# Kernel optimization log

Measured on AMD Instinct MI355X. Metric: run time of the kernel, lower is better.

Reference implementation:

```python
import jax, jax.numpy as jnp
import numpy as np

N = 50000       # nodes
E = 600000      # edges (avg degree 12)
F_IN = 64       # input_bands
F_HID = 128     # 2 * input_bands
F_OUT = 128     # output_bands
EPS = 1e-5      # BatchNorm eps


def setup_inputs() -> dict:
    key = jax.random.key(0)
    ks = jax.random.split(key, 12)
    x = jax.random.normal(ks[0], (N, F_IN), jnp.float32)
    edge_index = jax.random.randint(ks[1], (2, E), 0, N, dtype=jnp.int32)
    # GCNConv weight (glorot-ish) and bias
    W1 = jax.random.normal(ks[2], (F_IN, F_HID), jnp.float32) / np.sqrt(F_IN)
    b1 = jnp.zeros((F_HID,), jnp.float32)
    gamma1 = jnp.ones((F_HID,), jnp.float32)
    beta1 = jnp.zeros((F_HID,), jnp.float32)
    # SAGEConv: lin_l (aggregated neighbors, with bias), lin_r (root, no bias)
    Wl = jax.random.normal(ks[3], (F_HID, F_OUT), jnp.float32) / np.sqrt(F_HID)
    bl = jnp.zeros((F_OUT,), jnp.float32)
    Wr = jax.random.normal(ks[4], (F_HID, F_OUT), jnp.float32) / np.sqrt(F_HID)
    gamma2 = jnp.ones((F_OUT,), jnp.float32)
    beta2 = jnp.zeros((F_OUT,), jnp.float32)
    return {"x": x, "edge_index": edge_index, "W1": W1, "b1": b1,
            "gamma1": gamma1, "beta1": beta1, "Wl": Wl, "bl": bl,
            "Wr": Wr, "gamma2": gamma2, "beta2": beta2}


def _bn_train(h, gamma, beta):
    # BatchNorm1d in training mode: biased batch stats over the node axis
    mean = h.mean(axis=0)
    var = h.var(axis=0)
    return gamma * (h - mean) * jax.lax.rsqrt(var + EPS) + beta


def _gcn_conv(x, src, dst, W, b):
    # PyG GCNConv: x' = D^{-1/2}(A + I)D^{-1/2} X W + b
    h = x @ W                                   # [N, F_HID]
    loop = jnp.arange(N, dtype=src.dtype)
    src_sl = jnp.concatenate([src, loop])       # self-loops appended
    dst_sl = jnp.concatenate([dst, loop])
    deg = jax.ops.segment_sum(jnp.ones(E + N, h.dtype), dst_sl, num_segments=N)
    dis = jnp.where(deg > 0, jax.lax.rsqrt(deg), 0.0)  # deg^{-1/2}, inf -> 0
    norm = dis[src_sl] * dis[dst_sl]            # [E+N]
    msg = h[src_sl] * norm[:, None]             # gather + scale
    return jax.ops.segment_sum(msg, dst_sl, num_segments=N) + b


def _sage_conv(x, src, dst, Wl, bl, Wr):
    # PyG SAGEConv (mean aggr): x' = lin_l(mean_{j in N(i)} x_j) + lin_r(x_i)
    cnt = jax.ops.segment_sum(jnp.ones(E, x.dtype), dst, num_segments=N)
    neigh = jax.ops.segment_sum(x[src], dst, num_segments=N)
    neigh = neigh / jnp.maximum(cnt, 1.0)[:, None]
    return neigh @ Wl + bl + x @ Wr


def reference(x, edge_index, W1, b1, gamma1, beta1, Wl, bl, Wr, gamma2, beta2):
    src, dst = edge_index[0], edge_index[1]
    h = _gcn_conv(x, src, dst, W1, b1)
    h = jax.nn.relu(_bn_train(h, gamma1, beta1))  # dropout = identity (eval)
    h = _sage_conv(h, src, dst, Wl, bl, Wr)
    h = jax.nn.relu(_bn_train(h, gamma2, beta2))
    return h
```

## Files before the change

### kernel.cpp

```cpp
#include <hip/hip_runtime.h>


#define NN 50000
#define NE 600000
#define FIN 64
#define FHID 128
#define BN_EPS 1e-5f
#define CAP 64
#define NSLOT 32

typedef __attribute__((ext_vector_type(8))) short short8;
typedef __attribute__((ext_vector_type(4))) float f32x4;

__device__ __forceinline__ unsigned short f2bf(float f) {
  unsigned u = __float_as_uint(f);
  return (unsigned short)((u + 0x7FFFu + ((u >> 16) & 1u)) >> 16);
}
__device__ __forceinline__ float bfs(unsigned short u) {
  return __uint_as_float(((unsigned)u) << 16);
}
__device__ __forceinline__ float bflo(unsigned v) { return __uint_as_float(v << 16); }
__device__ __forceinline__ float bfhi(unsigned v) { return __uint_as_float(v & 0xFFFF0000u); }
__device__ __forceinline__ unsigned pk2(float lo, float hi) {
  return (unsigned)f2bf(lo) | ((unsigned)f2bf(hi) << 16);
}

__global__ __launch_bounds__(256) void bucket_fill(
    const int* __restrict__ src, const int* __restrict__ dst,
    int* __restrict__ cnt, int* __restrict__ csr,
    const float* __restrict__ W1, const float* __restrict__ Wl,
    const float* __restrict__ Wr, short* __restrict__ Wp1,
    short* __restrict__ Wp2, int nbE4) {
  int tid = threadIdx.x;
  if ((int)blockIdx.x < nbE4) {
    int e4 = blockIdx.x * 256 + tid;
    if (e4 * 4 < NE) {
      int4 d4 = ((const int4*)dst)[e4];
      int4 s4 = ((const int4*)src)[e4];
      int p;
      p = atomicAdd(&cnt[d4.x], 1); if (p < CAP) csr[(size_t)d4.x * CAP + p] = s4.x;
      p = atomicAdd(&cnt[d4.y], 1); if (p < CAP) csr[(size_t)d4.y * CAP + p] = s4.y;
      p = atomicAdd(&cnt[d4.z], 1); if (p < CAP) csr[(size_t)d4.z * CAP + p] = s4.z;
      p = atomicAdd(&cnt[d4.w], 1); if (p < CAP) csr[(size_t)d4.w * CAP + p] = s4.w;
    }
  } else {
    int widx = (blockIdx.x - nbE4) * 256 + tid;
    if (widx < 8192) {
      int kk = widx & 7, lane = (widx >> 3) & 63, ks = (widx >> 9) & 1,
          n = widx >> 10;
      int q = lane >> 4, r = lane & 15;
      int k = ks * 32 + q * 8 + kk, col = n * 16 + r;
      Wp1[widx] = (short)f2bf(W1[k * 128 + col]);
    } else if (widx < 8192 + 32768) {
      int w2 = widx - 8192;
      int kk = w2 & 7, lane = (w2 >> 3) & 63, ks = (w2 >> 9) & 7, n = w2 >> 12;
      int q = lane >> 4, r = lane & 15;
      int k = ks * 32 + q * 8 + kk, col = n * 16 + r;
      float wv = (k < 128) ? Wl[k * 128 + col] : Wr[(k - 128) * 128 + col];
      Wp2[w2] = (short)f2bf(wv);
    }
  }
}

__global__ __launch_bounds__(256) void scale_x(const float* __restrict__ x,
                                               const int* __restrict__ cnt,
                                               ushort4* __restrict__ xs,
                                               int* __restrict__ csr) {
  int i = blockIdx.x * 256 + threadIdx.x;
  float4 v = ((const float4*)x)[i];
  int node = i >> 4;
  float d = rsqrtf((float)(cnt[node] + 1));
  xs[i] = make_ushort4(f2bf(v.x * d), f2bf(v.y * d), f2bf(v.z * d), f2bf(v.w * d));
  if (i < NN) {
    int deg = min(cnt[i], CAP);
    int deg8 = (deg + 7) & ~7;
    int* cb = csr + (size_t)i * CAP;
    for (int p = deg; p < deg8; ++p) cb[p] = 0;
  }
}

__device__ __forceinline__ void gacc(float& a0, float& a1, float& a2, float& a3,
                                     ushort4 v) {
  a0 += bfs(v.x); a1 += bfs(v.y); a2 += bfs(v.z); a3 += bfs(v.w);
}

__global__ __launch_bounds__(256) void gcn_block(
    const unsigned short* __restrict__ xs, const int* __restrict__ csr,
    const int* __restrict__ cnt, const short* __restrict__ Wp1,
    const float* __restrict__ b1, unsigned short* __restrict__ hb,
    float* __restrict__ sums1s, float* __restrict__ sumsq1s) {
  __shared__ unsigned short xaS[16][72];
  __shared__ float lsum[128], lsq[128];
  int tid = threadIdx.x;
  if (tid < 128) { lsum[tid] = 0.f; lsq[tid] = 0.f; }
  int row_base = blockIdx.x * 16;
  int li = tid & 15, g = tid >> 4;
  int node = row_base + g;
  {
    int degr = cnt[node];
    int deg = min(degr, CAP);
    int deg8 = (deg + 7) & ~7;
    float di = rsqrtf((float)(degr + 1));
    ushort4 sv = *(const ushort4*)(xs + (size_t)node * FIN + li * 4);
    float a0 = bfs(sv.x), a1 = bfs(sv.y), a2 = bfs(sv.z), a3 = bfs(sv.w);
    ushort4 zv = *(const ushort4*)(xs + li * 4);
    const int* cb = csr + (size_t)node * CAP;
    int4 sA = *(const int4*)(cb);
    int4 sB = *(const int4*)(cb + 4);
    for (int e = 0; e < deg8; e += 8) {
      int pn = min(e + 8, CAP - 8);
      int4 nA = *(const int4*)(cb + pn);
      int4 nB = *(const int4*)(cb + pn + 4);
      ushort4 v0 = *(const ushort4*)(xs + (size_t)sA.x * FIN + li * 4);
      ushort4 v1 = *(const ushort4*)(xs + (size_t)sA.y * FIN + li * 4);
      ushort4 v2 = *(const ushort4*)(xs + (size_t)sA.z * FIN + li * 4);
      ushort4 v3 = *(const ushort4*)(xs + (size_t)sA.w * FIN + li * 4);
      ushort4 v4 = *(const ushort4*)(xs + (size_t)sB.x * FIN + li * 4);
      ushort4 v5 = *(const ushort4*)(xs + (size_t)sB.y * FIN + li * 4);
      ushort4 v6 = *(const ushort4*)(xs + (size_t)sB.z * FIN + li * 4);
      ushort4 v7 = *(const ushort4*)(xs + (size_t)sB.w * FIN + li * 4);
      gacc(a0, a1, a2, a3, v0); gacc(a0, a1, a2, a3, v1);
      gacc(a0, a1, a2, a3, v2); gacc(a0, a1, a2, a3, v3);
      gacc(a0, a1, a2, a3, v4); gacc(a0, a1, a2, a3, v5);
      gacc(a0, a1, a2, a3, v6); gacc(a0, a1, a2, a3, v7);
      sA = nA; sB = nB;
    }
    float pc = (float)(deg8 - deg);
    a0 -= pc * bfs(zv.x); a1 -= pc * bfs(zv.y);
    a2 -= pc * bfs(zv.z); a3 -= pc * bfs(zv.w);
    *(ushort4*)(&xaS[g][li * 4]) = make_ushort4(
        f2bf(di * a0), f2bf(di * a1), f2bf(di * a2), f2bf(di * a3));
  }
  __syncthreads();

  int lane = tid & 63, w = tid >> 6, r = lane & 15, q = lane >> 4;
  int n0 = w * 2, n1 = w * 2 + 1;
  short8 af0 = *(const short8*)(&xaS[r][q * 8]);
  short8 af1 = *(const short8*)(&xaS[r][32 + q * 8]);
  f32x4 acc0 = (f32x4){0.f, 0.f, 0.f, 0.f}, acc1 = acc0;
  acc0 = __builtin_amdgcn_mfma_f32_16x16x32_bf16(
      af0, *(const short8*)(Wp1 + ((size_t)(n0 * 2 + 0) * 64 + lane) * 8), acc0, 0, 0, 0);
  acc1 = __builtin_amdgcn_mfma_f32_16x16x32_bf16(
      af0, *(const short8*)(Wp1 + ((size_t)(n1 * 2 + 0) * 64 + lane) * 8), acc1, 0, 0, 0);
  acc0 = __builtin_amdgcn_mfma_f32_16x16x32_bf16(
      af1, *(const short8*)(Wp1 + ((size_t)(n0 * 2 + 1) * 64 + lane) * 8), acc0, 0, 0, 0);
  acc1 = __builtin_amdgcn_mfma_f32_16x16x32_bf16(
      af1, *(const short8*)(Wp1 + ((size_t)(n1 * 2 + 1) * 64 + lane) * 8), acc1, 0, 0, 0);

  float b0 = b1[n0 * 16 + r], bb1 = b1[n1 * 16 + r];
  float cs0 = 0.f, cq0 = 0.f, cs1 = 0.f, cq1 = 0.f;
#pragma unroll
  for (int i = 0; i < 4; ++i) {
    int row = row_base + q * 4 + i;
    float v0 = acc0[i] + b0;
    float v1 = acc1[i] + bb1;
    hb[(size_t)row * 128 + n0 * 16 + r] = f2bf(v0);
    hb[(size_t)row * 128 + n1 * 16 + r] = f2bf(v1);
    cs0 += v0; cq0 += v0 * v0;
    cs1 += v1; cq1 += v1 * v1;
  }
  atomicAdd(&lsum[n0 * 16 + r], cs0);
  atomicAdd(&lsq[n0 * 16 + r], cq0);
  atomicAdd(&lsum[n1 * 16 + r], cs1);
  atomicAdd(&lsq[n1 * 16 + r], cq1);
  __syncthreads();
  if (tid < 128) {
    int s = blockIdx.x & (NSLOT - 1);
    atomicAdd(&sums1s[s * 128 + tid], lsum[tid]);
    atomicAdd(&sumsq1s[s * 128 + tid], lsq[tid]);
  }
}

__global__ __launch_bounds__(256) void bn_slot_apply_bf(
    unsigned* __restrict__ hb, const float* __restrict__ sums1s,
    const float* __restrict__ sumsq1s, const float* __restrict__ gamma,
    const float* __restrict__ beta) {
  __shared__ float sc[128], sh[128];
  int t = threadIdx.x;
  if (t < 128) {
    float ms = 0.f, vs = 0.f;
#pragma unroll
    for (int s = 0; s < NSLOT; ++s) {
      ms += sums1s[s * 128 + t];
      vs += sumsq1s[s * 128 + t];
    }
    float mean = ms * (1.0f / NN);
    float var = fmaxf(vs * (1.0f / NN) - mean * mean, 0.f);
    float sgm = gamma[t] * rsqrtf(var + BN_EPS);
    sc[t] = sgm;
    sh[t] = beta[t] - mean * sgm;
  }
  __syncthreads();
  for (int i = blockIdx.x * 256 + t; i < NN * FHID / 4; i += gridDim.x * 256) {
    uint2 v = ((uint2*)hb)[i];
    int c = (i & 31) * 4;
    float f0 = fmaxf(fmaf(bflo(v.x), sc[c + 0], sh[c + 0]), 0.f);
    float f1 = fmaxf(fmaf(bfhi(v.x), sc[c + 1], sh[c + 1]), 0.f);
    float f2 = fmaxf(fmaf(bflo(v.y), sc[c + 2], sh[c + 2]), 0.f);
    float f3 = fmaxf(fmaf(bfhi(v.y), sc[c + 3], sh[c + 3]), 0.f);
    v.x = pk2(f0, f1);
    v.y = pk2(f2, f3);
    ((uint2*)hb)[i] = v;
  }
}

__device__ __forceinline__ void sacc(float* a, uint4 v) {
  a[0] += bflo(v.x); a[1] += bfhi(v.x);
  a[2] += bflo(v.y); a[3] += bfhi(v.y);
  a[4] += bflo(v.z); a[5] += bfhi(v.z);
  a[6] += bflo(v.w); a[7] += bfhi(v.w);
}

__global__ __launch_bounds__(256) void sage_block(
    const unsigned short* __restrict__ hb, const int* __restrict__ csr,
    const int* __restrict__ cnt, const short* __restrict__ Wp2,
    const float* __restrict__ bl, float* __restrict__ out,
    float* __restrict__ sums2s, float* __restrict__ sumsq2s) {
  __shared__ unsigned short nbS[16][136];
  __shared__ float lsum[128], lsq[128];
  int tid = threadIdx.x;
  if (tid < 128) { lsum[tid] = 0.f; lsq[tid] = 0.f; }
  int row_base = blockIdx.x * 16;
  int li = tid & 15, g = tid >> 4;
  int node = row_base + g;
  const unsigned* hbu = (const unsigned*)hb;
  {
    int degr = cnt[node];
    int deg = min(degr, CAP);
    int deg8 = (deg + 7) & ~7;
    float a[8];
#pragma unroll
    for (int j = 0; j < 8; ++j) a[j] = 0.f;
    uint4 zv = *(const uint4*)(hbu + li * 4);
    const int* cb = csr + (size_t)node * CAP;
    int4 sA = *(const int4*)(cb);
    int4 sB = *(const int4*)(cb + 4);
    for (int e = 0; e < deg8; e += 8) {
      int pn = min(e + 8, CAP - 8);
      int4 nA = *(const int4*)(cb + pn);
      int4 nB = *(const int4*)(cb + pn + 4);
      uint4 v0 = *(const uint4*)(hbu + (size_t)sA.x * 64 + li * 4);
      uint4 v1 = *(const uint4*)(hbu + (size_t)sA.y * 64 + li * 4);
      uint4 v2 = *(const uint4*)(hbu + (size_t)sA.z * 64 + li * 4);
      uint4 v3 = *(const uint4*)(hbu + (size_t)sA.w * 64 + li * 4);
      uint4 v4 = *(const uint4*)(hbu + (size_t)sB.x * 64 + li * 4);
      uint4 v5 = *(const uint4*)(hbu + (size_t)sB.y * 64 + li * 4);
      uint4 v6 = *(const uint4*)(hbu + (size_t)sB.z * 64 + li * 4);
      uint4 v7 = *(const uint4*)(hbu + (size_t)sB.w * 64 + li * 4);
      sacc(a, v0); sacc(a, v1); sacc(a, v2); sacc(a, v3);
      sacc(a, v4); sacc(a, v5); sacc(a, v6); sacc(a, v7);
      sA = nA; sB = nB;
    }
    float pc = (float)(deg8 - deg);
    a[0] -= pc * bflo(zv.x); a[1] -= pc * bfhi(zv.x);
    a[2] -= pc * bflo(zv.y); a[3] -= pc * bfhi(zv.y);
    a[4] -= pc * bflo(zv.z); a[5] -= pc * bfhi(zv.z);
    a[6] -= pc * bflo(zv.w); a[7] -= pc * bfhi(zv.w);
    float inv = 1.0f / fmaxf((float)degr, 1.0f);
    uint4 o;
    o.x = pk2(a[0] * inv, a[1] * inv);
    o.y = pk2(a[2] * inv, a[3] * inv);
    o.z = pk2(a[4] * inv, a[5] * inv);
    o.w = pk2(a[6] * inv, a[7] * inv);
    *(uint4*)(&nbS[g][li * 8]) = o;
  }
  __syncthreads();

  int lane = tid & 63, w = tid >> 6, r = lane & 15, q = lane >> 4;
  int n0 = w * 2, n1 = w * 2 + 1;
  short8 af[8];
#pragma unroll
  for (int ks = 0; ks < 4; ++ks)
    af[ks] = *(const short8*)(&nbS[r][ks * 32 + q * 8]);
  int rowg = row_base + r;
#pragma unroll
  for (int ks = 4; ks < 8; ++ks) {
    int kg = (ks - 4) * 32 + q * 8;
    af[ks] = *(const short8*)((const short*)hb + (size_t)rowg * 128 + kg);
  }
  f32x4 acc0 = (f32x4){0.f, 0.f, 0.f, 0.f}, acc1 = acc0;
#pragma unroll
  for (int ks = 0; ks < 8; ++ks) {
    acc0 = __builtin_amdgcn_mfma_f32_16x16x32_bf16(
        af[ks], *(const short8*)(Wp2 + ((size_t)(n0 * 8 + ks) * 64 + lane) * 8),
        acc0, 0, 0, 0);
    acc1 = __builtin_amdgcn_mfma_f32_16x16x32_bf16(
        af[ks], *(const short8*)(Wp2 + ((size_t)(n1 * 8 + ks) * 64 + lane) * 8),
        acc1, 0, 0, 0);
  }

  float b0 = bl[n0 * 16 + r], bb1 = bl[n1 * 16 + r];
  float cs0 = 0.f, cq0 = 0.f, cs1 = 0.f, cq1 = 0.f;
#pragma unroll
  for (int i = 0; i < 4; ++i) {
    int row = row_base + q * 4 + i;
    float v0 = acc0[i] + b0;
    float v1 = acc1[i] + bb1;
    out[(size_t)row * 128 + n0 * 16 + r] = v0;
    out[(size_t)row * 128 + n1 * 16 + r] = v1;
    cs0 += v0; cq0 += v0 * v0;
    cs1 += v1; cq1 += v1 * v1;
  }
  atomicAdd(&lsum[n0 * 16 + r], cs0);
  atomicAdd(&lsq[n0 * 16 + r], cq0);
  atomicAdd(&lsum[n1 * 16 + r], cs1);
  atomicAdd(&lsq[n1 * 16 + r], cq1);
  __syncthreads();
  if (tid < 128) {
    int s = blockIdx.x & (NSLOT - 1);
    atomicAdd(&sums2s[s * 128 + tid], lsum[tid]);
    atomicAdd(&sumsq2s[s * 128 + tid], lsq[tid]);
  }
}

__global__ __launch_bounds__(256) void bn_slot_apply_f32(
    float* __restrict__ out, const float* __restrict__ sums2s,
    const float* __restrict__ sumsq2s, const float* __restrict__ gamma,
    const float* __restrict__ beta) {
  __shared__ float sc[128], sh[128];
  int t = threadIdx.x;
  if (t < 128) {
    float ms = 0.f, vs = 0.f;
#pragma unroll
    for (int s = 0; s < NSLOT; ++s) {
      ms += sums2s[s * 128 + t];
      vs += sumsq2s[s * 128 + t];
    }
    float mean = ms * (1.0f / NN);
    float var = fmaxf(vs * (1.0f / NN) - mean * mean, 0.f);
    float sgm = gamma[t] * rsqrtf(var + BN_EPS);
    sc[t] = sgm;
    sh[t] = beta[t] - mean * sgm;
  }
  __syncthreads();
  for (int i4 = blockIdx.x * 256 + t; i4 < NN * FHID / 4; i4 += gridDim.x * 256) {
    float4 v = ((const float4*)out)[i4];
    int f = (i4 & 31) * 4;
    v.x = fmaxf(fmaf(v.x, sc[f + 0], sh[f + 0]), 0.f);
    v.y = fmaxf(fmaf(v.y, sc[f + 1], sh[f + 1]), 0.f);
    v.z = fmaxf(fmaf(v.z, sc[f + 2], sh[f + 2]), 0.f);
    v.w = fmaxf(fmaf(v.w, sc[f + 3], sh[f + 3]), 0.f);
    ((float4*)out)[i4] = v;
  }
}

extern "C" void kernel_launch(void* const* d_in, const int* in_sizes, int n_in,
                              void* d_out, int out_size, void* d_ws, size_t ws_size,
                              hipStream_t stream) {
  const float* x   = (const float*)d_in[0];
  const int*   ei  = (const int*)d_in[1];
  const float* W1  = (const float*)d_in[2];
  const float* b1  = (const float*)d_in[3];
  const float* g1  = (const float*)d_in[4];
  const float* be1 = (const float*)d_in[5];
  const float* Wl  = (const float*)d_in[6];
  const float* bl  = (const float*)d_in[7];
  const float* Wr  = (const float*)d_in[8];
  const float* g2  = (const float*)d_in[9];
  const float* be2 = (const float*)d_in[10];
  const int* srcp = ei;
  const int* dstp = ei + NE;

  char* w = (char*)d_ws;
  auto alloc = [&](size_t bytes) {
    char* p = w;
    w += (bytes + 255) & ~(size_t)255;
    return p;
  };
  size_t zbytes = ((size_t)NN + 4 * NSLOT * 128) * 4;
  char* zz = (char*)alloc(zbytes);
  int*   cnt   = (int*)zz;
  float* stats = (float*)(cnt + NN);
  float* sums1s = stats,                     *sumsq1s = stats + NSLOT * 128;
  float* sums2s = stats + 2 * NSLOT * 128,   *sumsq2s = stats + 3 * NSLOT * 128;

  int*   csr = (int*)alloc((size_t)NN * CAP * 4);
  unsigned short* xs = (unsigned short*)alloc((size_t)NN * FIN * 2);
  unsigned short* hb = (unsigned short*)alloc((size_t)NN * FHID * 2);
  short* Wp1 = (short*)alloc(8192 * 2);
  short* Wp2 = (short*)alloc(32768 * 2);

  hipMemsetAsync(zz, 0, zbytes, stream);

  int nbE4 = (NE / 4 + 255) / 256;
  int nbW  = (8192 + 32768 + 255) / 256;
  int nb16 = NN / 16;

  bucket_fill<<<nbE4 + nbW, 256, 0, stream>>>(srcp, dstp, cnt, csr, W1, Wl, Wr,
                                              Wp1, Wp2, nbE4);
  scale_x<<<NN * FIN / 4 / 256, 256, 0, stream>>>(x, cnt, (ushort4*)xs, csr);
  gcn_block<<<nb16, 256, 0, stream>>>(xs, csr, cnt, Wp1, b1, hb, sums1s, sumsq1s);
  bn_slot_apply_bf<<<512, 256, 0, stream>>>((unsigned*)hb, sums1s, sumsq1s, g1, be1);
  sage_block<<<nb16, 256, 0, stream>>>(hb, csr, cnt, Wp2, bl, (float*)d_out,
                                       sums2s, sumsq2s);
  bn_slot_apply_f32<<<512, 256, 0, stream>>>((float*)d_out, sums2s, sumsq2s, g2, be2);
}
```

Baseline: 215.3 us.

## Fold x bf16 conversion into build kernel and apply source degree norm in gather

The separate scale_x kernel is removed. x is now converted to bf16 unscaled inside the combined build kernel, and the CSR zero-padding pass is dropped. The GCN gather loads cnt[src] per neighbour and applies rsqrt(deg+1) on the fly, with a masked tail block replacing the padded-slot correction. This saves a kernel launch and a dependent pass over x, at the cost of an extra random 4-byte gather and rsqrt per edge in the GCN aggregation.

```diff
diff --git a/kernel.cpp b/kernel.cpp
--- a/kernel.cpp
+++ b/kernel.cpp
@@ -25,15 +25,16 @@
   return (unsigned)f2bf(lo) | ((unsigned)f2bf(hi) << 16);
 }
 
-__global__ __launch_bounds__(256) void bucket_fill(
+__global__ __launch_bounds__(256) void build_all(
     const int* __restrict__ src, const int* __restrict__ dst,
-    int* __restrict__ cnt, int* __restrict__ csr,
+    const float* __restrict__ x, int* __restrict__ cnt, int* __restrict__ csr,
     const float* __restrict__ W1, const float* __restrict__ Wl,
     const float* __restrict__ Wr, short* __restrict__ Wp1,
-    short* __restrict__ Wp2, int nbE4) {
+    short* __restrict__ Wp2, ushort4* __restrict__ xsr, int nbE4, int nbW) {
   int tid = threadIdx.x;
-  if ((int)blockIdx.x < nbE4) {
-    int e4 = blockIdx.x * 256 + tid;
+  int b = blockIdx.x;
+  if (b < nbE4) {
+    int e4 = b * 256 + tid;
     if (e4 * 4 < NE) {
       int4 d4 = ((const int4*)dst)[e4];
       int4 s4 = ((const int4*)src)[e4];
@@ -43,8 +44,8 @@
       p = atomicAdd(&cnt[d4.z], 1); if (p < CAP) csr[(size_t)d4.z * CAP + p] = s4.z;
       p = atomicAdd(&cnt[d4.w], 1); if (p < CAP) csr[(size_t)d4.w * CAP + p] = s4.w;
     }
-  } else {
-    int widx = (blockIdx.x - nbE4) * 256 + tid;
+  } else if (b < nbE4 + nbW) {
+    int widx = (b - nbE4) * 256 + tid;
     if (widx < 8192) {
       int kk = widx & 7, lane = (widx >> 3) & 63, ks = (widx >> 9) & 1,
           n = widx >> 10;
@@ -59,29 +60,11 @@
       float wv = (k < 128) ? Wl[k * 128 + col] : Wr[(k - 128) * 128 + col];
       Wp2[w2] = (short)f2bf(wv);
     }
-  }
-}
-
-__global__ __launch_bounds__(256) void scale_x(const float* __restrict__ x,
-                                               const int* __restrict__ cnt,
-                                               ushort4* __restrict__ xs,
-                                               int* __restrict__ csr) {
-  int i = blockIdx.x * 256 + threadIdx.x;
-  float4 v = ((const float4*)x)[i];
-  int node = i >> 4;
-  float d = rsqrtf((float)(cnt[node] + 1));
-  xs[i] = make_ushort4(f2bf(v.x * d), f2bf(v.y * d), f2bf(v.z * d), f2bf(v.w * d));
-  if (i < NN) {
-    int deg = min(cnt[i], CAP);
-    int deg8 = (deg + 7) & ~7;
-    int* cb = csr + (size_t)i * CAP;
-    for (int p = deg; p < deg8; ++p) cb[p] = 0;
-  }
-}
-
-__device__ __forceinline__ void gacc(float& a0, float& a1, float& a2, float& a3,
-                                     ushort4 v) {
-  a0 += bfs(v.x); a1 += bfs(v.y); a2 += bfs(v.z); a3 += bfs(v.w);
+  } else {
+    int i = (b - nbE4 - nbW) * 256 + tid;
+    float4 v = ((const float4*)x)[i];
+    xsr[i] = make_ushort4(f2bf(v.x), f2bf(v.y), f2bf(v.z), f2bf(v.w));
+  }
 }
 
 __global__ __launch_bounds__(256) void gcn_block(
@@ -98,19 +81,29 @@
   int node = row_base + g;
   {
     int degr = cnt[node];
-    int deg = min(degr, CAP);
-    int deg8 = (deg + 7) & ~7;
+    int degc = min(degr, CAP);
     float di = rsqrtf((float)(degr + 1));
     ushort4 sv = *(const ushort4*)(xs + (size_t)node * FIN + li * 4);
-    float a0 = bfs(sv.x), a1 = bfs(sv.y), a2 = bfs(sv.z), a3 = bfs(sv.w);
+    float a0 = di * bfs(sv.x), a1 = di * bfs(sv.y);
+    float a2 = di * bfs(sv.z), a3 = di * bfs(sv.w);
+    float dis0 = rsqrtf((float)(cnt[0] + 1));
     ushort4 zv = *(const ushort4*)(xs + li * 4);
     const int* cb = csr + (size_t)node * CAP;
     int4 sA = *(const int4*)(cb);
     int4 sB = *(const int4*)(cb + 4);
-    for (int e = 0; e < deg8; e += 8) {
+    int e = 0;
+    for (; e + 8 <= degc; e += 8) {
       int pn = min(e + 8, CAP - 8);
       int4 nA = *(const int4*)(cb + pn);
       int4 nB = *(const int4*)(cb + pn + 4);
+      float d0 = rsqrtf((float)(cnt[sA.x] + 1));
+      float d1 = rsqrtf((float)(cnt[sA.y] + 1));
+      float d2 = rsqrtf((float)(cnt[sA.z] + 1));
+      float d3 = rsqrtf((float)(cnt[sA.w] + 1));
+      float d4 = rsqrtf((float)(cnt[sB.x] + 1));
+      float d5 = rsqrtf((float)(cnt[sB.y] + 1));
+      float d6 = rsqrtf((float)(cnt[sB.z] + 1));
+      float d7 = rsqrtf((float)(cnt[sB.w] + 1));
       ushort4 v0 = *(const ushort4*)(xs + (size_t)sA.x * FIN + li * 4);
       ushort4 v1 = *(const ushort4*)(xs + (size_t)sA.y * FIN + li * 4);
       ushort4 v2 = *(const ushort4*)(xs + (size_t)sA.z * FIN + li * 4);
@@ -119,15 +112,50 @@
       ushort4 v5 = *(const ushort4*)(xs + (size_t)sB.y * FIN + li * 4);
       ushort4 v6 = *(const ushort4*)(xs + (size_t)sB.z * FIN + li * 4);
       ushort4 v7 = *(const ushort4*)(xs + (size_t)sB.w * FIN + li * 4);
-      gacc(a0, a1, a2, a3, v0); gacc(a0, a1, a2, a3, v1);
-      gacc(a0, a1, a2, a3, v2); gacc(a0, a1, a2, a3, v3);
-      gacc(a0, a1, a2, a3, v4); gacc(a0, a1, a2, a3, v5);
-      gacc(a0, a1, a2, a3, v6); gacc(a0, a1, a2, a3, v7);
+      a0 += d0 * bfs(v0.x); a1 += d0 * bfs(v0.y); a2 += d0 * bfs(v0.z); a3 += d0 * bfs(v0.w);
+      a0 += d1 * bfs(v1.x); a1 += d1 * bfs(v1.y); a2 += d1 * bfs(v1.z); a3 += d1 * bfs(v1.w);
+      a0 += d2 * bfs(v2.x); a1 += d2 * bfs(v2.y); a2 += d2 * bfs(v2.z); a3 += d2 * bfs(v2.w);
+      a0 += d3 * bfs(v3.x); a1 += d3 * bfs(v3.y); a2 += d3 * bfs(v3.z); a3 += d3 * bfs(v3.w);
+      a0 += d4 * bfs(v4.x); a1 += d4 * bfs(v4.y); a2 += d4 * bfs(v4.z); a3 += d4 * bfs(v4.w);
+      a0 += d5 * bfs(v5.x); a1 += d5 * bfs(v5.y); a2 += d5 * bfs(v5.z); a3 += d5 * bfs(v5.w);
+      a0 += d6 * bfs(v6.x); a1 += d6 * bfs(v6.y); a2 += d6 * bfs(v6.z); a3 += d6 * bfs(v6.w);
+      a0 += d7 * bfs(v7.x); a1 += d7 * bfs(v7.y); a2 += d7 * bfs(v7.z); a3 += d7 * bfs(v7.w);
       sA = nA; sB = nB;
     }
-    float pc = (float)(deg8 - deg);
-    a0 -= pc * bfs(zv.x); a1 -= pc * bfs(zv.y);
-    a2 -= pc * bfs(zv.z); a3 -= pc * bfs(zv.w);
+    int rem = degc - e;
+    if (rem) {
+      int i0 = (0 < rem) ? sA.x : 0, i1 = (1 < rem) ? sA.y : 0;
+      int i2 = (2 < rem) ? sA.z : 0, i3 = (3 < rem) ? sA.w : 0;
+      int i4 = (4 < rem) ? sB.x : 0, i5 = (5 < rem) ? sB.y : 0;
+      int i6 = (6 < rem) ? sB.z : 0, i7 = (7 < rem) ? sB.w : 0;
+      float d0 = rsqrtf((float)(cnt[i0] + 1));
+      float d1 = rsqrtf((float)(cnt[i1] + 1));
+      float d2 = rsqrtf((float)(cnt[i2] + 1));
+      float d3 = rsqrtf((float)(cnt[i3] + 1));
+      float d4 = rsqrtf((float)(cnt[i4] + 1));
+      float d5 = rsqrtf((float)(cnt[i5] + 1));
+      float d6 = rsqrtf((float)(cnt[i6] + 1));
+      float d7 = rsqrtf((float)(cnt[i7] + 1));
+      ushort4 v0 = *(const ushort4*)(xs + (size_t)i0 * FIN + li * 4);
+      ushort4 v1 = *(const ushort4*)(xs + (size_t)i1 * FIN + li * 4);
+      ushort4 v2 = *(const ushort4*)(xs + (size_t)i2 * FIN + li * 4);
+      ushort4 v3 = *(const ushort4*)(xs + (size_t)i3 * FIN + li * 4);
+      ushort4 v4 = *(const ushort4*)(xs + (size_t)i4 * FIN + li * 4);
+      ushort4 v5 = *(const ushort4*)(xs + (size_t)i5 * FIN + li * 4);
+      ushort4 v6 = *(const ushort4*)(xs + (size_t)i6 * FIN + li * 4);
+      ushort4 v7 = *(const ushort4*)(xs + (size_t)i7 * FIN + li * 4);
+      a0 += d0 * bfs(v0.x); a1 += d0 * bfs(v0.y); a2 += d0 * bfs(v0.z); a3 += d0 * bfs(v0.w);
+      a0 += d1 * bfs(v1.x); a1 += d1 * bfs(v1.y); a2 += d1 * bfs(v1.z); a3 += d1 * bfs(v1.w);
+      a0 += d2 * bfs(v2.x); a1 += d2 * bfs(v2.y); a2 += d2 * bfs(v2.z); a3 += d2 * bfs(v2.w);
+      a0 += d3 * bfs(v3.x); a1 += d3 * bfs(v3.y); a2 += d3 * bfs(v3.z); a3 += d3 * bfs(v3.w);
+      a0 += d4 * bfs(v4.x); a1 += d4 * bfs(v4.y); a2 += d4 * bfs(v4.z); a3 += d4 * bfs(v4.w);
+      a0 += d5 * bfs(v5.x); a1 += d5 * bfs(v5.y); a2 += d5 * bfs(v5.z); a3 += d5 * bfs(v5.w);
+      a0 += d6 * bfs(v6.x); a1 += d6 * bfs(v6.y); a2 += d6 * bfs(v6.z); a3 += d6 * bfs(v6.w);
+      a0 += d7 * bfs(v7.x); a1 += d7 * bfs(v7.y); a2 += d7 * bfs(v7.z); a3 += d7 * bfs(v7.w);
+      float pc = (float)(8 - rem) * dis0;
+      a0 -= pc * bfs(zv.x); a1 -= pc * bfs(zv.y);
+      a2 -= pc * bfs(zv.z); a3 -= pc * bfs(zv.w);
+    }
     *(ushort4*)(&xaS[g][li * 4]) = make_ushort4(
         f2bf(di * a0), f2bf(di * a1), f2bf(di * a2), f2bf(di * a3));
   }
@@ -226,8 +254,7 @@
   const unsigned* hbu = (const unsigned*)hb;
   {
     int degr = cnt[node];
-    int deg = min(degr, CAP);
-    int deg8 = (deg + 7) & ~7;
+    int degc = min(degr, CAP);
     float a[8];
 #pragma unroll
     for (int j = 0; j < 8; ++j) a[j] = 0.f;
@@ -235,7 +262,8 @@
     const int* cb = csr + (size_t)node * CAP;
     int4 sA = *(const int4*)(cb);
     int4 sB = *(const int4*)(cb + 4);
-    for (int e = 0; e < deg8; e += 8) {
+    int e = 0;
+    for (; e + 8 <= degc; e += 8) {
       int pn = min(e + 8, CAP - 8);
       int4 nA = *(const int4*)(cb + pn);
       int4 nB = *(const int4*)(cb + pn + 4);
@@ -251,11 +279,28 @@
       sacc(a, v4); sacc(a, v5); sacc(a, v6); sacc(a, v7);
       sA = nA; sB = nB;
     }
-    float pc = (float)(deg8 - deg);
-    a[0] -= pc * bflo(zv.x); a[1] -= pc * bfhi(zv.x);
-    a[2] -= pc * bflo(zv.y); a[3] -= pc * bfhi(zv.y);
-    a[4] -= pc * bflo(zv.z); a[5] -= pc * bfhi(zv.z);
-    a[6] -= pc * bflo(zv.w); a[7] -= pc * bfhi(zv.w);
+    int rem = degc - e;
+    if (rem) {
+      int i0 = (0 < rem) ? sA.x : 0, i1 = (1 < rem) ? sA.y : 0;
+      int i2 = (2 < rem) ? sA.z : 0, i3 = (3 < rem) ? sA.w : 0;
+      int i4 = (4 < rem) ? sB.x : 0, i5 = (5 < rem) ? sB.y : 0;
+      int i6 = (6 < rem) ? sB.z : 0, i7 = (7 < rem) ? sB.w : 0;
+      uint4 v0 = *(const uint4*)(hbu + (size_t)i0 * 64 + li * 4);
+      uint4 v1 = *(const uint4*)(hbu + (size_t)i1 * 64 + li * 4);
+      uint4 v2 = *(const uint4*)(hbu + (size_t)i2 * 64 + li * 4);
+      uint4 v3 = *(const uint4*)(hbu + (size_t)i3 * 64 + li * 4);
+      uint4 v4 = *(const uint4*)(hbu + (size_t)i4 * 64 + li * 4);
+      uint4 v5 = *(const uint4*)(hbu + (size_t)i5 * 64 + li * 4);
+      uint4 v6 = *(const uint4*)(hbu + (size_t)i6 * 64 + li * 4);
+      uint4 v7 = *(const uint4*)(hbu + (size_t)i7 * 64 + li * 4);
+      sacc(a, v0); sacc(a, v1); sacc(a, v2); sacc(a, v3);
+      sacc(a, v4); sacc(a, v5); sacc(a, v6); sacc(a, v7);
+      float pc = (float)(8 - rem);
+      a[0] -= pc * bflo(zv.x); a[1] -= pc * bfhi(zv.x);
+      a[2] -= pc * bflo(zv.y); a[3] -= pc * bfhi(zv.y);
+      a[4] -= pc * bflo(zv.z); a[5] -= pc * bfhi(zv.z);
+      a[6] -= pc * bflo(zv.w); a[7] -= pc * bfhi(zv.w);
+    }
     float inv = 1.0f / fmaxf((float)degr, 1.0f);
     uint4 o;
     o.x = pk2(a[0] * inv, a[1] * inv);
@@ -384,11 +429,11 @@
 
   int nbE4 = (NE / 4 + 255) / 256;
   int nbW  = (8192 + 32768 + 255) / 256;
+  int nbX  = NN * FIN / 4 / 256;
   int nb16 = NN / 16;
 
-  bucket_fill<<<nbE4 + nbW, 256, 0, stream>>>(srcp, dstp, cnt, csr, W1, Wl, Wr,
-                                              Wp1, Wp2, nbE4);
-  scale_x<<<NN * FIN / 4 / 256, 256, 0, stream>>>(x, cnt, (ushort4*)xs, csr);
+  build_all<<<nbE4 + nbW + nbX, 256, 0, stream>>>(
+      srcp, dstp, x, cnt, csr, W1, Wl, Wr, Wp1, Wp2, (ushort4*)xs, nbE4, nbW);
   gcn_block<<<nb16, 256, 0, stream>>>(xs, csr, cnt, Wp1, b1, hb, sums1s, sumsq1s);
   bn_slot_apply_bf<<<512, 256, 0, stream>>>((unsigned*)hb, sums1s, sumsq1s, g1, be1);
   sage_block<<<nb16, 256, 0, stream>>>(hb, csr, cnt, Wp2, bl, (float*)d_out,
```

Measured after the change: 218.7 us. About the same (+1.6%).
